# Kernel optimization log

Hardware: AMD Instinct MI355X
Metric: run time of the kernel (lower is better)

Reference implementation:

```python
import jax, jax.numpy as jnp
import numpy as np

N_NODES = 100000
N_EDGES = 1600000
INP, EMB, OUT = 8, 64, 1
N_LAYERS = 4


def setup_inputs() -> dict:
    key = jax.random.key(0)
    ks = jax.random.split(key, 16)
    s = lambda fan_in: 1.0 / np.sqrt(fan_in)
    inp = {
        "x": jax.random.normal(ks[0], (N_NODES, INP), jnp.float32),
        "edge_index": jax.random.randint(ks[1], (2, N_EDGES), 0, N_NODES, jnp.int32),
        "edge_weight": jax.random.uniform(ks[2], (N_EDGES,), jnp.float32),
        # encoder MLP: Linear(INP,EMB) -> ReLU -> Linear(EMB,EMB)
        "enc_w1": jax.random.uniform(ks[3], (INP, EMB), jnp.float32, -s(INP), s(INP)),
        "enc_b1": jnp.zeros((EMB,), jnp.float32),
        "enc_w2": jax.random.uniform(ks[4], (EMB, EMB), jnp.float32, -s(EMB), s(EMB)),
        "enc_b2": jnp.zeros((EMB,), jnp.float32),
        # stacked GCNConv weights/biases
        "gcn_w": jax.random.uniform(ks[5], (N_LAYERS, EMB, EMB), jnp.float32, -s(EMB), s(EMB)),
        "gcn_b": jnp.zeros((N_LAYERS, EMB), jnp.float32),
        # decoder MLP: Linear(EMB,EMB) -> ReLU -> Linear(EMB,OUT)
        "dec_w1": jax.random.uniform(ks[6], (EMB, EMB), jnp.float32, -s(EMB), s(EMB)),
        "dec_b1": jnp.zeros((EMB,), jnp.float32),
        "dec_w2": jax.random.uniform(ks[7], (EMB, OUT), jnp.float32, -s(EMB), s(EMB)),
        "dec_b2": jnp.zeros((OUT,), jnp.float32),
    }
    return inp


def _gcn_norm(edge_index, edge_weight, n_nodes):
    # PyG gcn_norm with add_self_loops=True, symmetric normalization.
    loop = jnp.arange(n_nodes, dtype=edge_index.dtype)
    src = jnp.concatenate([edge_index[0], loop])
    dst = jnp.concatenate([edge_index[1], loop])
    w = jnp.concatenate([edge_weight, jnp.ones((n_nodes,), edge_weight.dtype)])
    deg = jax.ops.segment_sum(w, dst, num_segments=n_nodes)
    dis = jnp.where(deg > 0, jax.lax.rsqrt(jnp.where(deg > 0, deg, 1.0)), 0.0)
    norm = dis[src] * w * dis[dst]  # [E + N]
    return src, dst, norm


def reference(x, edge_index, edge_weight, enc_w1, enc_b1, enc_w2, enc_b2,
              gcn_w, gcn_b, dec_w1, dec_b1, dec_w2, dec_b2):
    n_nodes = x.shape[0]
    src, dst, norm = _gcn_norm(edge_index, edge_weight, n_nodes)

    # encoder MLP
    h = jax.nn.relu(x @ enc_w1 + enc_b1) @ enc_w2 + enc_b2  # [N, EMB]

    # message passing: GCNConv then ReLU, per layer
    for i in range(gcn_w.shape[0]):
        t = h @ gcn_w[i]                             # linear transform [N, EMB]
        msg = norm[:, None] * t[src]                 # gather + weight [E+N, EMB]
        agg = jax.ops.segment_sum(msg, dst, num_segments=n_nodes)
        h = jax.nn.relu(agg + gcn_b[i])

    # decoder MLP
    out = jax.nn.relu(h @ dec_w1 + dec_b1) @ dec_w2 + dec_b2  # [N, OUT]
    return out
```

## Files before the change

### kernel.cpp

```cpp
#include <hip/hip_runtime.h>


constexpr int NN   = 100000;
constexpr int NE   = 1600000;
constexpr int INPD = 8;
constexpr int EMBD = 64;
constexpr int NLAY = 4;
constexpr float FPSCALE = 16777216.0f;
constexpr int LNODES = 32;
constexpr int BNODES = 256;
constexpr int NBUCK  = (NN + BNODES - 1) / BNODES;
constexpr int BCAP   = 5120;
constexpr int ACHUNK = 12288;
constexpr int ABLOCKS = (NE + ACHUNK - 1) / ACHUNK;

__global__ void k_zero(int* bcnt) {
    int i = blockIdx.x * blockDim.x + threadIdx.x;
    if (i < NBUCK) bcnt[i] = 0;
}

__global__ __launch_bounds__(1024) void k_passA(const int* __restrict__ ei,
                                                const float* __restrict__ w,
                                                int* __restrict__ bcnt,
                                                int2* __restrict__ brec) {
    __shared__ int lcnt[NBUCK];
    __shared__ int lbase[NBUCK];
    int tid = threadIdx.x;
    int beg = blockIdx.x * ACHUNK;
    int end = beg + ACHUNK; if (end > NE) end = NE;

    for (int i = tid; i < NBUCK; i += 1024) lcnt[i] = 0;
    __syncthreads();
    for (int e = beg + tid; e < end; e += 1024)
        atomicAdd(&lcnt[ei[NE + e] >> 8], 1);
    __syncthreads();
    for (int i = tid; i < NBUCK; i += 1024) {
        int c = lcnt[i];
        lbase[i] = (c > 0) ? atomicAdd(&bcnt[i], c) : 0;
        lcnt[i] = 0;
    }
    __syncthreads();
    for (int e = beg + tid; e < end; e += 1024) {
        int s = ei[e];
        int d = ei[NE + e];
        int b = d >> 8, dl = d & 255;
        int pos = lbase[b] + atomicAdd(&lcnt[b], 1);
        if (pos < BCAP)
            brec[(size_t)b * BCAP + pos] = make_int2(s | (dl << 17), __float_as_int(w[e]));
    }
}

__global__ __launch_bounds__(512) void k_bscan(const int* __restrict__ bcnt,
                                               int* __restrict__ bucket_base,
                                               int* __restrict__ row_ptr) {
    __shared__ int s[512];
    int tid = threadIdx.x;
    int v = (tid < NBUCK) ? bcnt[tid] : 0;
    s[tid] = v;
    __syncthreads();
    for (int off = 1; off < 512; off <<= 1) {
        int t = (tid >= off) ? s[tid - off] : 0;
        __syncthreads();
        s[tid] += t;
        __syncthreads();
    }
    if (tid < NBUCK) bucket_base[tid + 1] = s[tid];
    if (tid == 0) { bucket_base[0] = 0; row_ptr[NN] = NE; }
}

__global__ __launch_bounds__(256) void k_passB(const int2* __restrict__ brec,
                                               const int* __restrict__ bcnt,
                                               const int* __restrict__ bucket_base,
                                               float* __restrict__ dis,
                                               int* __restrict__ row_ptr,
                                               int2* __restrict__ csr) {
    __shared__ int2 sbuf[BCAP];
    __shared__ unsigned int sdeg[BNODES];
    __shared__ int scnt[BNODES];
    __shared__ int sincl[BNODES];
    __shared__ int scur[BNODES];
    int b = blockIdx.x;
    int tid = threadIdx.x;
    int n = bcnt[b]; if (n > BCAP) n = BCAP;
    int nodes = NN - b * BNODES; if (nodes > BNODES) nodes = BNODES;
    const int2* rec = brec + (size_t)b * BCAP;

    sdeg[tid] = 0; scnt[tid] = 0;
    __syncthreads();
    for (int i = tid; i < n; i += 256) {
        int2 r = rec[i];
        int dl = (r.x >> 17) & 255;
        unsigned int fx = (unsigned int)(__int_as_float(r.y) * FPSCALE + 0.5f);
        atomicAdd(&sdeg[dl], fx);
        atomicAdd(&scnt[dl], 1);
    }
    __syncthreads();
    sincl[tid] = scnt[tid];
    __syncthreads();
    for (int off = 1; off < 256; off <<= 1) {
        int t = (tid >= off) ? sincl[tid - off] : 0;
        __syncthreads();
        sincl[tid] += t;
        __syncthreads();
    }
    int excl = sincl[tid] - scnt[tid];
    scur[tid] = excl;
    int base = bucket_base[b];
    if (tid < nodes) {
        float deg = 1.0f + (float)sdeg[tid] * (1.0f / FPSCALE);
        dis[b * BNODES + tid] = 1.0f / sqrtf(deg);
        row_ptr[b * BNODES + tid] = base + excl;
    }
    __syncthreads();
    for (int i = tid; i < n; i += 256) {
        int2 r = rec[i];
        int dl = (r.x >> 17) & 255;
        int p = atomicAdd(&scur[dl], 1);
        sbuf[p] = r;
    }
    __syncthreads();
    for (int i = tid; i < n; i += 256) csr[base + i] = sbuf[i];
}

__global__ __launch_bounds__(256) void k_norm(const int* __restrict__ bucket_base,
                                              const float* __restrict__ dis,
                                              int2* __restrict__ csr) {
    int b = blockIdx.x;
    int tid = threadIdx.x;
    int base = bucket_base[b];
    int n = bucket_base[b + 1] - base;
    for (int i = tid; i < n; i += 256) {
        int2 r = csr[base + i];
        int s = r.x & 0x1FFFF;
        int dl = (r.x >> 17) & 255;
        float v = dis[s] * __int_as_float(r.y) * dis[b * BNODES + dl];
        csr[base + i] = make_int2(r.x, __float_as_int(v));
    }
}

__global__ __launch_bounds__(256) void k_encoder(const float* __restrict__ x,
                                                 const float* __restrict__ w1,
                                                 const float* __restrict__ b1,
                                                 const float* __restrict__ w2,
                                                 const float* __restrict__ b2,
                                                 float* __restrict__ h) {
    __shared__ float sW1[INPD * EMBD];
    __shared__ float sW2[EMBD * EMBD];
    __shared__ float sB1[EMBD];
    __shared__ float sB2[EMBD];
    __shared__ float sZ[16][EMBD];
    int tid = threadIdx.x;
    for (int i = tid; i < INPD * EMBD; i += 256) sW1[i] = w1[i];
    for (int i = tid; i < EMBD * EMBD; i += 256) sW2[i] = w2[i];
    if (tid < EMBD) { sB1[tid] = b1[tid]; sB2[tid] = b2[tid]; }
    __syncthreads();
    int base = blockIdx.x * 16;
    #pragma unroll
    for (int it = 0; it < 4; ++it) {
        int item = tid + it * 256;
        int nl = item >> 6, j = item & 63;
        int node = base + nl;
        float acc = sB1[j];
        if (node < NN) {
            const float* xr = x + (size_t)node * INPD;
            #pragma unroll
            for (int k = 0; k < INPD; ++k) acc += xr[k] * sW1[k * EMBD + j];
        }
        sZ[nl][j] = fmaxf(acc, 0.0f);
    }
    __syncthreads();
    #pragma unroll
    for (int it = 0; it < 4; ++it) {
        int item = tid + it * 256;
        int nl = item >> 6, j2 = item & 63;
        int node = base + nl;
        if (node < NN) {
            float acc = sB2[j2];
            for (int j = 0; j < EMBD; ++j) acc += sZ[nl][j] * sW2[j * EMBD + j2];
            h[(size_t)node * EMBD + j2] = acc;
        }
    }
}

__global__ __launch_bounds__(512) void k_layer(const float* __restrict__ hin,
                                               const float* __restrict__ dis,
                                               const int* __restrict__ row_ptr,
                                               const int2* __restrict__ edges,
                                               const float* __restrict__ W,
                                               const float* __restrict__ bias,
                                               float* __restrict__ hout) {
    __shared__ float sW[EMBD * EMBD];
    __shared__ float sB[EMBD];
    __shared__ float sA[LNODES][EMBD];
    int tid = threadIdx.x;
    for (int i = tid; i < EMBD * EMBD; i += 512) sW[i] = W[i];
    if (tid < EMBD) sB[tid] = bias[tid];

    int g = tid >> 4, l = tid & 15;
    int node = blockIdx.x * LNODES + g;
    const float4* h4 = (const float4*)hin;
    float4 a0 = make_float4(0.f, 0.f, 0.f, 0.f);
    float4 a1 = a0, a2 = a0, a3 = a0;
    if (node < NN) {
        float dsn = dis[node];
        float sn = dsn * dsn;
        a0 = h4[(size_t)node * 16 + l];
        a0.x *= sn; a0.y *= sn; a0.z *= sn; a0.w *= sn;
        int beg = row_ptr[node], end = row_ptr[node + 1];
        int e = beg;
        for (; e + 4 <= end; e += 4) {
            int2 e0 = edges[e], e1 = edges[e + 1], e2 = edges[e + 2], e3 = edges[e + 3];
            float4 t0 = h4[(size_t)(e0.x & 0x1FFFF) * 16 + l];
            float4 t1 = h4[(size_t)(e1.x & 0x1FFFF) * 16 + l];
            float4 t2 = h4[(size_t)(e2.x & 0x1FFFF) * 16 + l];
            float4 t3 = h4[(size_t)(e3.x & 0x1FFFF) * 16 + l];
            float v0 = __int_as_float(e0.y), v1 = __int_as_float(e1.y);
            float v2 = __int_as_float(e2.y), v3 = __int_as_float(e3.y);
            a0.x += v0 * t0.x; a0.y += v0 * t0.y; a0.z += v0 * t0.z; a0.w += v0 * t0.w;
            a1.x += v1 * t1.x; a1.y += v1 * t1.y; a1.z += v1 * t1.z; a1.w += v1 * t1.w;
            a2.x += v2 * t2.x; a2.y += v2 * t2.y; a2.z += v2 * t2.z; a2.w += v2 * t2.w;
            a3.x += v3 * t3.x; a3.y += v3 * t3.y; a3.z += v3 * t3.z; a3.w += v3 * t3.w;
        }
        for (; e < end; ++e) {
            int2 ev = edges[e];
            float v = __int_as_float(ev.y);
            float4 tv = h4[(size_t)(ev.x & 0x1FFFF) * 16 + l];
            a0.x += v * tv.x; a0.y += v * tv.y; a0.z += v * tv.z; a0.w += v * tv.w;
        }
    }
    a0.x += a1.x + a2.x + a3.x;
    a0.y += a1.y + a2.y + a3.y;
    a0.z += a1.z + a2.z + a3.z;
    a0.w += a1.w + a2.w + a3.w;
    ((float4*)&sA[g][0])[l] = a0;
    __syncthreads();

    int base = blockIdx.x * LNODES;
    #pragma unroll
    for (int it = 0; it < 4; ++it) {
        int item = tid + it * 512;
        int nl = item >> 6, j2 = item & 63;
        int onode = base + nl;
        if (onode < NN) {
            float o = sB[j2];
            for (int k = 0; k < EMBD; ++k) o += sA[nl][k] * sW[k * EMBD + j2];
            hout[(size_t)onode * EMBD + j2] = fmaxf(o, 0.0f);
        }
    }
}

__global__ __launch_bounds__(256) void k_decoder(const float* __restrict__ h,
                                                 const float* __restrict__ w1,
                                                 const float* __restrict__ b1,
                                                 const float* __restrict__ w2,
                                                 const float* __restrict__ b2,
                                                 float* __restrict__ out) {
    __shared__ float sW1[EMBD * EMBD];
    __shared__ float sB1[EMBD];
    __shared__ float sW2[EMBD];
    int tid = threadIdx.x;
    for (int i = tid; i < EMBD * EMBD; i += 256) sW1[i] = w1[i];
    if (tid < EMBD) { sB1[tid] = b1[tid]; sW2[tid] = w2[tid]; }
    __syncthreads();
    int wave = tid >> 6, lane = tid & 63;
    float db2 = b2[0];
    #pragma unroll
    for (int it = 0; it < 4; ++it) {
        int node = blockIdx.x * 16 + wave * 4 + it;
        if (node >= NN) continue;
        const float* hr = h + (size_t)node * EMBD;
        float acc = sB1[lane];
        for (int k = 0; k < EMBD; ++k) acc += hr[k] * sW1[k * EMBD + lane];
        acc = fmaxf(acc, 0.0f);
        float r = acc * sW2[lane];
        for (int o = 32; o > 0; o >>= 1) r += __shfl_down(r, o);
        if (lane == 0) out[node] = r + db2;
    }
}

extern "C" void kernel_launch(void* const* d_in, const int* in_sizes, int n_in,
                              void* d_out, int out_size, void* d_ws, size_t ws_size,
                              hipStream_t stream) {
    const float* x      = (const float*)d_in[0];
    const int*   ei     = (const int*)  d_in[1];
    const float* ew     = (const float*)d_in[2];
    const float* enc_w1 = (const float*)d_in[3];
    const float* enc_b1 = (const float*)d_in[4];
    const float* enc_w2 = (const float*)d_in[5];
    const float* enc_b2 = (const float*)d_in[6];
    const float* gcn_w  = (const float*)d_in[7];
    const float* gcn_b  = (const float*)d_in[8];
    const float* dec_w1 = (const float*)d_in[9];
    const float* dec_b1 = (const float*)d_in[10];
    const float* dec_w2 = (const float*)d_in[11];
    const float* dec_b2 = (const float*)d_in[12];
    float* out = (float*)d_out;

    char* ws = (char*)d_ws;
    size_t off = 0;
    auto alloc = [&](size_t bytes) -> void* {
        void* p = (void*)(ws + off);
        off += (bytes + 511) & ~(size_t)511;
        return p;
    };
    int*   bcnt        = (int*)  alloc(NBUCK * 4);
    int*   bucket_base = (int*)  alloc((NBUCK + 1) * 4);
    int2*  brec        = (int2*) alloc((size_t)NBUCK * BCAP * 8);
    float* dis         = (float*)alloc(NN * 4);
    int*   row_ptr     = (int*)  alloc((NN + 1) * 4);
    int2*  csr         = (int2*) alloc((size_t)NE * 8);
    float* hbuf        = (float*)alloc((size_t)NN * EMBD * 4);
    float* hbuf2       = (float*)alloc((size_t)NN * EMBD * 4);
    (void)ws_size; (void)n_in; (void)in_sizes; (void)out_size;

    int gT16 = (NN + 15) / 16;
    int gL   = (NN + LNODES - 1) / LNODES;

    k_zero<<<(NBUCK + 255) / 256, 256, 0, stream>>>(bcnt);
    k_passA<<<ABLOCKS, 1024, 0, stream>>>(ei, ew, bcnt, brec);
    k_bscan<<<1, 512, 0, stream>>>(bcnt, bucket_base, row_ptr);
    k_passB<<<NBUCK, 256, 0, stream>>>(brec, bcnt, bucket_base, dis, row_ptr, csr);
    k_norm<<<NBUCK, 256, 0, stream>>>(bucket_base, dis, csr);

    k_encoder<<<gT16, 256, 0, stream>>>(x, enc_w1, enc_b1, enc_w2, enc_b2, hbuf);

    float* cur = hbuf;
    float* nxt = hbuf2;
    for (int layer = 0; layer < NLAY; ++layer) {
        k_layer<<<gL, 512, 0, stream>>>(cur, dis, row_ptr, csr,
                                        gcn_w + (size_t)layer * EMBD * EMBD,
                                        gcn_b + (size_t)layer * EMBD, nxt);
        float* tmp = cur; cur = nxt; nxt = tmp;
    }

    k_decoder<<<gT16, 256, 0, stream>>>(cur, dec_w1, dec_b1, dec_w2, dec_b2, out);
}
```

Baseline: 501.7 us.

## Fuse decoder into last GCN layer and make bucket scatter deterministic

The fourth GCN layer and the decoder MLP now run in one kernel, so the final hidden state never goes to global memory and is not read back. Edge bucketing is reworked into a per-block histogram, a column scan and a scatter at precomputed offsets, which removes the global atomics and the zeroing kernel. The encoder now handles 32 nodes per block. The trade is two extra small launches in preprocessing, a larger histogram buffer, and higher shared-memory use in the fused kernel.

```diff
diff --git a/kernel.cpp b/kernel.cpp
--- a/kernel.cpp
+++ b/kernel.cpp
@@ -5,42 +5,79 @@
 constexpr int NE   = 1600000;
 constexpr int INPD = 8;
 constexpr int EMBD = 64;
-constexpr int NLAY = 4;
 constexpr float FPSCALE = 16777216.0f;
 constexpr int LNODES = 32;
 constexpr int BNODES = 256;
 constexpr int NBUCK  = (NN + BNODES - 1) / BNODES;
 constexpr int BCAP   = 5120;
-constexpr int ACHUNK = 12288;
-constexpr int ABLOCKS = (NE + ACHUNK - 1) / ACHUNK;
-
-__global__ void k_zero(int* bcnt) {
-    int i = blockIdx.x * blockDim.x + threadIdx.x;
-    if (i < NBUCK) bcnt[i] = 0;
-}
-
-__global__ __launch_bounds__(1024) void k_passA(const int* __restrict__ ei,
-                                                const float* __restrict__ w,
-                                                int* __restrict__ bcnt,
-                                                int2* __restrict__ brec) {
+constexpr int NBLKA  = 512;
+constexpr int CHUNKA = (NE + NBLKA - 1) / NBLKA;
+
+__global__ __launch_bounds__(512) void k_hist(const int* __restrict__ ei,
+                                              int* __restrict__ hist) {
     __shared__ int lcnt[NBUCK];
+    int tid = threadIdx.x;
+    int beg = blockIdx.x * CHUNKA;
+    int end = beg + CHUNKA; if (end > NE) end = NE;
+    for (int i = tid; i < NBUCK; i += 512) lcnt[i] = 0;
+    __syncthreads();
+    for (int e = beg + tid; e < end; e += 512)
+        atomicAdd(&lcnt[ei[NE + e] >> 8], 1);
+    __syncthreads();
+    for (int i = tid; i < NBUCK; i += 512) hist[blockIdx.x * NBUCK + i] = lcnt[i];
+}
+
+__global__ __launch_bounds__(512) void k_colscan(int* __restrict__ hist,
+                                                 int* __restrict__ totals) {
+    __shared__ int s[512];
+    int j = blockIdx.x;
+    int b = threadIdx.x;
+    int v = hist[b * NBUCK + j];
+    s[b] = v;
+    __syncthreads();
+    for (int off = 1; off < 512; off <<= 1) {
+        int t = (b >= off) ? s[b - off] : 0;
+        __syncthreads();
+        s[b] += t;
+        __syncthreads();
+    }
+    hist[b * NBUCK + j] = s[b] - v;
+    if (b == 511) totals[j] = s[b];
+}
+
+__global__ __launch_bounds__(512) void k_bscan(const int* __restrict__ totals,
+                                               int* __restrict__ bucket_base,
+                                               int* __restrict__ row_ptr) {
+    __shared__ int s[512];
+    int tid = threadIdx.x;
+    int v = (tid < NBUCK) ? totals[tid] : 0;
+    s[tid] = v;
+    __syncthreads();
+    for (int off = 1; off < 512; off <<= 1) {
+        int t = (tid >= off) ? s[tid - off] : 0;
+        __syncthreads();
+        s[tid] += t;
+        __syncthreads();
+    }
+    if (tid < NBUCK) bucket_base[tid + 1] = s[tid];
+    if (tid == 0) { bucket_base[0] = 0; row_ptr[NN] = NE; }
+}
+
+__global__ __launch_bounds__(512) void k_scatter(const int* __restrict__ ei,
+                                                 const float* __restrict__ w,
+                                                 const int* __restrict__ hist,
+                                                 int2* __restrict__ brec) {
     __shared__ int lbase[NBUCK];
-    int tid = threadIdx.x;
-    int beg = blockIdx.x * ACHUNK;
-    int end = beg + ACHUNK; if (end > NE) end = NE;
-
-    for (int i = tid; i < NBUCK; i += 1024) lcnt[i] = 0;
-    __syncthreads();
-    for (int e = beg + tid; e < end; e += 1024)
-        atomicAdd(&lcnt[ei[NE + e] >> 8], 1);
-    __syncthreads();
-    for (int i = tid; i < NBUCK; i += 1024) {
-        int c = lcnt[i];
-        lbase[i] = (c > 0) ? atomicAdd(&bcnt[i], c) : 0;
+    __shared__ int lcnt[NBUCK];
+    int tid = threadIdx.x;
+    int beg = blockIdx.x * CHUNKA;
+    int end = beg + CHUNKA; if (end > NE) end = NE;
+    for (int i = tid; i < NBUCK; i += 512) {
+        lbase[i] = hist[blockIdx.x * NBUCK + i];
         lcnt[i] = 0;
     }
     __syncthreads();
-    for (int e = beg + tid; e < end; e += 1024) {
+    for (int e = beg + tid; e < end; e += 512) {
         int s = ei[e];
         int d = ei[NE + e];
         int b = d >> 8, dl = d & 255;
@@ -50,26 +87,8 @@
     }
 }
 
-__global__ __launch_bounds__(512) void k_bscan(const int* __restrict__ bcnt,
-                                               int* __restrict__ bucket_base,
-                                               int* __restrict__ row_ptr) {
-    __shared__ int s[512];
-    int tid = threadIdx.x;
-    int v = (tid < NBUCK) ? bcnt[tid] : 0;
-    s[tid] = v;
-    __syncthreads();
-    for (int off = 1; off < 512; off <<= 1) {
-        int t = (tid >= off) ? s[tid - off] : 0;
-        __syncthreads();
-        s[tid] += t;
-        __syncthreads();
-    }
-    if (tid < NBUCK) bucket_base[tid + 1] = s[tid];
-    if (tid == 0) { bucket_base[0] = 0; row_ptr[NN] = NE; }
-}
-
 __global__ __launch_bounds__(256) void k_passB(const int2* __restrict__ brec,
-                                               const int* __restrict__ bcnt,
+                                               const int* __restrict__ totals,
                                                const int* __restrict__ bucket_base,
                                                float* __restrict__ dis,
                                                int* __restrict__ row_ptr,
@@ -81,7 +100,7 @@
     __shared__ int scur[BNODES];
     int b = blockIdx.x;
     int tid = threadIdx.x;
-    int n = bcnt[b]; if (n > BCAP) n = BCAP;
+    int n = totals[b]; if (n > BCAP) n = BCAP;
     int nodes = NN - b * BNODES; if (nodes > BNODES) nodes = BNODES;
     const int2* rec = brec + (size_t)b * BCAP;
 
@@ -148,15 +167,15 @@
     __shared__ float sW2[EMBD * EMBD];
     __shared__ float sB1[EMBD];
     __shared__ float sB2[EMBD];
-    __shared__ float sZ[16][EMBD];
+    __shared__ float sZ[32][EMBD];
     int tid = threadIdx.x;
     for (int i = tid; i < INPD * EMBD; i += 256) sW1[i] = w1[i];
     for (int i = tid; i < EMBD * EMBD; i += 256) sW2[i] = w2[i];
     if (tid < EMBD) { sB1[tid] = b1[tid]; sB2[tid] = b2[tid]; }
     __syncthreads();
-    int base = blockIdx.x * 16;
-    #pragma unroll
-    for (int it = 0; it < 4; ++it) {
+    int base = blockIdx.x * 32;
+    #pragma unroll
+    for (int it = 0; it < 8; ++it) {
         int item = tid + it * 256;
         int nl = item >> 6, j = item & 63;
         int node = base + nl;
@@ -170,7 +189,7 @@
     }
     __syncthreads();
     #pragma unroll
-    for (int it = 0; it < 4; ++it) {
+    for (int it = 0; it < 8; ++it) {
         int item = tid + it * 256;
         int nl = item >> 6, j2 = item & 63;
         int node = base + nl;
@@ -249,33 +268,108 @@
     }
 }
 
-__global__ __launch_bounds__(256) void k_decoder(const float* __restrict__ h,
-                                                 const float* __restrict__ w1,
-                                                 const float* __restrict__ b1,
-                                                 const float* __restrict__ w2,
-                                                 const float* __restrict__ b2,
-                                                 float* __restrict__ out) {
-    __shared__ float sW1[EMBD * EMBD];
-    __shared__ float sB1[EMBD];
-    __shared__ float sW2[EMBD];
-    int tid = threadIdx.x;
-    for (int i = tid; i < EMBD * EMBD; i += 256) sW1[i] = w1[i];
-    if (tid < EMBD) { sB1[tid] = b1[tid]; sW2[tid] = w2[tid]; }
-    __syncthreads();
-    int wave = tid >> 6, lane = tid & 63;
-    float db2 = b2[0];
+__global__ __launch_bounds__(512) void k_layer_dec(const float* __restrict__ hin,
+                                                   const float* __restrict__ dis,
+                                                   const int* __restrict__ row_ptr,
+                                                   const int2* __restrict__ edges,
+                                                   const float* __restrict__ W,
+                                                   const float* __restrict__ bias,
+                                                   const float* __restrict__ w1d,
+                                                   const float* __restrict__ b1d,
+                                                   const float* __restrict__ w2d,
+                                                   const float* __restrict__ b2d,
+                                                   float* __restrict__ out) {
+    __shared__ float sW[EMBD * EMBD];
+    __shared__ float sW1d[EMBD * EMBD];
+    __shared__ float sB[EMBD];
+    __shared__ float sB1d[EMBD];
+    __shared__ float sW2d[EMBD];
+    __shared__ float sA[LNODES][EMBD];
+    int tid = threadIdx.x;
+    for (int i = tid; i < EMBD * EMBD; i += 512) { sW[i] = W[i]; sW1d[i] = w1d[i]; }
+    if (tid < EMBD) { sB[tid] = bias[tid]; sB1d[tid] = b1d[tid]; sW2d[tid] = w2d[tid]; }
+
+    int g = tid >> 4, l = tid & 15;
+    int node = blockIdx.x * LNODES + g;
+    const float4* h4 = (const float4*)hin;
+    float4 a0 = make_float4(0.f, 0.f, 0.f, 0.f);
+    float4 a1 = a0, a2 = a0, a3 = a0;
+    if (node < NN) {
+        float dsn = dis[node];
+        float sn = dsn * dsn;
+        a0 = h4[(size_t)node * 16 + l];
+        a0.x *= sn; a0.y *= sn; a0.z *= sn; a0.w *= sn;
+        int beg = row_ptr[node], end = row_ptr[node + 1];
+        int e = beg;
+        for (; e + 4 <= end; e += 4) {
+            int2 e0 = edges[e], e1 = edges[e + 1], e2 = edges[e + 2], e3 = edges[e + 3];
+            float4 t0 = h4[(size_t)(e0.x & 0x1FFFF) * 16 + l];
+            float4 t1 = h4[(size_t)(e1.x & 0x1FFFF) * 16 + l];
+            float4 t2 = h4[(size_t)(e2.x & 0x1FFFF) * 16 + l];
+            float4 t3 = h4[(size_t)(e3.x & 0x1FFFF) * 16 + l];
+            float v0 = __int_as_float(e0.y), v1 = __int_as_float(e1.y);
+            float v2 = __int_as_float(e2.y), v3 = __int_as_float(e3.y);
+            a0.x += v0 * t0.x; a0.y += v0 * t0.y; a0.z += v0 * t0.z; a0.w += v0 * t0.w;
+            a1.x += v1 * t1.x; a1.y += v1 * t1.y; a1.z += v1 * t1.z; a1.w += v1 * t1.w;
+            a2.x += v2 * t2.x; a2.y += v2 * t2.y; a2.z += v2 * t2.z; a2.w += v2 * t2.w;
+            a3.x += v3 * t3.x; a3.y += v3 * t3.y; a3.z += v3 * t3.z; a3.w += v3 * t3.w;
+        }
+        for (; e < end; ++e) {
+            int2 ev = edges[e];
+            float v = __int_as_float(ev.y);
+            float4 tv = h4[(size_t)(ev.x & 0x1FFFF) * 16 + l];
+            a0.x += v * tv.x; a0.y += v * tv.y; a0.z += v * tv.z; a0.w += v * tv.w;
+        }
+    }
+    a0.x += a1.x + a2.x + a3.x;
+    a0.y += a1.y + a2.y + a3.y;
+    a0.z += a1.z + a2.z + a3.z;
+    a0.w += a1.w + a2.w + a3.w;
+    ((float4*)&sA[g][0])[l] = a0;
+    __syncthreads();
+
+    float hv[4];
     #pragma unroll
     for (int it = 0; it < 4; ++it) {
-        int node = blockIdx.x * 16 + wave * 4 + it;
-        if (node >= NN) continue;
-        const float* hr = h + (size_t)node * EMBD;
-        float acc = sB1[lane];
-        for (int k = 0; k < EMBD; ++k) acc += hr[k] * sW1[k * EMBD + lane];
-        acc = fmaxf(acc, 0.0f);
-        float r = acc * sW2[lane];
-        for (int o = 32; o > 0; o >>= 1) r += __shfl_down(r, o);
-        if (lane == 0) out[node] = r + db2;
-    }
+        int item = tid + it * 512;
+        int nl = item >> 6, j2 = item & 63;
+        float o = sB[j2];
+        for (int k = 0; k < EMBD; ++k) o += sA[nl][k] * sW[k * EMBD + j2];
+        hv[it] = fmaxf(o, 0.0f);
+    }
+    __syncthreads();
+    #pragma unroll
+    for (int it = 0; it < 4; ++it) {
+        int item = tid + it * 512;
+        sA[item >> 6][item & 63] = hv[it];
+    }
+    __syncthreads();
+
+    float zv[4];
+    #pragma unroll
+    for (int it = 0; it < 4; ++it) {
+        int item = tid + it * 512;
+        int nl = item >> 6, j2 = item & 63;
+        float o = sB1d[j2];
+        for (int k = 0; k < EMBD; ++k) o += sA[nl][k] * sW1d[k * EMBD + j2];
+        zv[it] = fmaxf(o, 0.0f);
+    }
+    __syncthreads();
+    #pragma unroll
+    for (int it = 0; it < 4; ++it) {
+        int item = tid + it * 512;
+        sA[item >> 6][item & 63] = zv[it];
+    }
+    __syncthreads();
+
+    float r = 0.0f;
+    #pragma unroll
+    for (int u = 0; u < 4; ++u) r += sA[g][l * 4 + u] * sW2d[l * 4 + u];
+    r += __shfl_xor(r, 1);
+    r += __shfl_xor(r, 2);
+    r += __shfl_xor(r, 4);
+    r += __shfl_xor(r, 8);
+    if (l == 0 && node < NN) out[node] = r + b2d[0];
 }
 
 extern "C" void kernel_launch(void* const* d_in, const int* in_sizes, int n_in,
@@ -303,7 +397,8 @@
         off += (bytes + 511) & ~(size_t)511;
         return p;
     };
-    int*   bcnt        = (int*)  alloc(NBUCK * 4);
+    int*   hist        = (int*)  alloc((size_t)NBLKA * NBUCK * 4);
+    int*   totals      = (int*)  alloc(NBUCK * 4);
     int*   bucket_base = (int*)  alloc((NBUCK + 1) * 4);
     int2*  brec        = (int2*) alloc((size_t)NBUCK * BCAP * 8);
     float* dis         = (float*)alloc(NN * 4);
@@ -313,25 +408,28 @@
     float* hbuf2       = (float*)alloc((size_t)NN * EMBD * 4);
     (void)ws_size; (void)n_in; (void)in_sizes; (void)out_size;
 
-    int gT16 = (NN + 15) / 16;
+    int gE32 = (NN + 31) / 32;
     int gL   = (NN + LNODES - 1) / LNODES;
 
-    k_zero<<<(NBUCK + 255) / 256, 256, 0, stream>>>(bcnt);
-    k_passA<<<ABLOCKS, 1024, 0, stream>>>(ei, ew, bcnt, brec);
-    k_bscan<<<1, 512, 0, stream>>>(bcnt, bucket_base, row_ptr);
-    k_passB<<<NBUCK, 256, 0, stream>>>(brec, bcnt, bucket_base, dis, row_ptr, csr);
+    k_hist<<<NBLKA, 512, 0, stream>>>(ei, hist);
+    k_colscan<<<NBUCK, 512, 0, stream>>>(hist, totals);
+    k_bscan<<<1, 512, 0, stream>>>(totals, bucket_base, row_ptr);
+    k_scatter<<<NBLKA, 512, 0, stream>>>(ei, ew, hist, brec);
+    k_passB<<<NBUCK, 256, 0, stream>>>(brec, totals, bucket_base, dis, row_ptr, csr);
     k_norm<<<NBUCK, 256, 0, stream>>>(bucket_base, dis, csr);
 
-    k_encoder<<<gT16, 256, 0, stream>>>(x, enc_w1, enc_b1, enc_w2, enc_b2, hbuf);
+    k_encoder<<<gE32, 256, 0, stream>>>(x, enc_w1, enc_b1, enc_w2, enc_b2, hbuf);
 
     float* cur = hbuf;
     float* nxt = hbuf2;
-    for (int layer = 0; layer < NLAY; ++layer) {
+    for (int layer = 0; layer < 3; ++layer) {
         k_layer<<<gL, 512, 0, stream>>>(cur, dis, row_ptr, csr,
                                         gcn_w + (size_t)layer * EMBD * EMBD,
                                         gcn_b + (size_t)layer * EMBD, nxt);
         float* tmp = cur; cur = nxt; nxt = tmp;
     }
-
-    k_decoder<<<gT16, 256, 0, stream>>>(cur, dec_w1, dec_b1, dec_w2, dec_b2, out);
-}
+    k_layer_dec<<<gL, 512, 0, stream>>>(cur, dis, row_ptr, csr,
+                                        gcn_w + (size_t)3 * EMBD * EMBD,
+                                        gcn_b + (size_t)3 * EMBD,
+                                        dec_w1, dec_b1, dec_w2, dec_b2, out);
+}
```

New measurement: 444.6 us. 11.4% less time.
